# Optimization experiments

Hardware: AMD Instinct MI355X
Metric: run time of the kernel (lower is better)

Reference implementation:

```python
import jax, jax.numpy as jnp
import numpy as np

NUM_EXPERTS = 8
TOP_K = 2
HIDDEN = 2048
INTER = 1408
NUM_TOKENS = 8192


def setup_inputs() -> dict:
    key = jax.random.key(0)
    k1, k2, k3, k4 = jax.random.split(key, 4)
    hidden_states = jax.random.normal(k1, (NUM_TOKENS, HIDDEN), dtype=jnp.float32)
    router_weight = jax.random.normal(k2, (NUM_EXPERTS, HIDDEN), dtype=jnp.float32) * 0.02
    gate_up_proj = jax.random.normal(k3, (NUM_EXPERTS, 2 * INTER, HIDDEN), dtype=jnp.float32) * 0.02
    down_proj = jax.random.normal(k4, (NUM_EXPERTS, HIDDEN, INTER), dtype=jnp.float32) * 0.02
    return {
        "hidden_states": hidden_states,
        "router_weight": router_weight,
        "gate_up_proj": gate_up_proj,
        "down_proj": down_proj,
    }


def reference(hidden_states, router_weight, gate_up_proj, down_proj):
    T, H = hidden_states.shape
    E = router_weight.shape[0]
    dtype = hidden_states.dtype

    # Router: logits -> fp32 softmax -> top-k -> normalize -> cast back
    logits = hidden_states @ router_weight.T                      # [T, E]
    probs = jax.nn.softmax(logits.astype(jnp.float32), axis=-1)
    rw, sel = jax.lax.top_k(probs, TOP_K)                          # [T, K]
    rw = rw / jnp.sum(rw, axis=-1, keepdims=True)                  # norm_topk_prob=True
    rw = rw.astype(dtype)

    # Dense combine weights per token per expert (zero for unselected experts)
    combine = jnp.zeros((T, E), dtype=dtype)
    combine = combine.at[jnp.arange(T)[:, None], sel].add(rw)      # [T, E]

    out = jnp.zeros_like(hidden_states)
    for e in range(E):  # small fixed loop over experts
        gate_up = hidden_states @ gate_up_proj[e].T                # [T, 2I]
        gate, up = jnp.split(gate_up, 2, axis=-1)
        h = jax.nn.silu(gate) * up                                 # SiluAndMul
        expert_out = h @ down_proj[e].T                            # [T, H]
        out = out + combine[:, e:e + 1] * expert_out
    return out
```

## Files before the change

### kernel.cpp

```cpp
#include <hip/hip_runtime.h>
#include <hip/hip_bf16.h>
#include <stdint.h>
#include <math.h>


#define E_ 8
#define H_ 2048
#define I_ 1408
#define T_ 8192
#define NSLOT (T_ * 2)
#define NBLK 64
#define G1S 408
#define G2S 272
#define G1 (8 * G1S)
#define G2 (8 * G2S)

typedef __bf16 bf16;
typedef bf16 bf16x4 __attribute__((ext_vector_type(4)));
typedef bf16 bf16x8 __attribute__((ext_vector_type(8)));
typedef float f32x4 __attribute__((ext_vector_type(4)));

__device__ inline void gl2lds16(const void* g, void* l) {
  __builtin_amdgcn_global_load_lds(
      (const __attribute__((address_space(1))) unsigned int*)g,
      (__attribute__((address_space(3))) unsigned int*)l, 16, 0, 0);
}

__global__ __launch_bounds__(256) void cvtw_k(const float* __restrict__ a, int n8a,
                                              const float* __restrict__ b, int n8b,
                                              bf16* __restrict__ oa,
                                              bf16* __restrict__ ob) {
  int stride = gridDim.x * blockDim.x;
  int ntot = n8a + n8b;
  for (int i = blockIdx.x * blockDim.x + threadIdx.x; i < ntot; i += stride) {
    const float* src; bf16* dst; int k;
    if (i < n8a) { src = a; dst = oa; k = i; }
    else         { src = b; dst = ob; k = i - n8a; }
    const float4* p = (const float4*)src + (size_t)k * 2;
    float4 x = p[0], y = p[1];
    bf16x8 o;
    o[0] = (bf16)x.x; o[1] = (bf16)x.y; o[2] = (bf16)x.z; o[3] = (bf16)x.w;
    o[4] = (bf16)y.x; o[5] = (bf16)y.y; o[6] = (bf16)y.z; o[7] = (bf16)y.w;
    *((bf16x8*)dst + k) = o;
  }
}

__global__ __launch_bounds__(256) void router_k(const float* __restrict__ X,
                                                const float* __restrict__ R,
                                                bf16* __restrict__ xbf,
                                                int* __restrict__ sel,
                                                float* __restrict__ wts) {
  int lane = threadIdx.x & 63;
  int t = blockIdx.x * 4 + (threadIdx.x >> 6);
  const float4* x4 = (const float4*)(X + (size_t)t * H_);
  bf16x4* xb4 = (bf16x4*)(xbf + (size_t)t * H_);
  float acc[E_];
#pragma unroll
  for (int e = 0; e < E_; ++e) acc[e] = 0.f;
#pragma unroll
  for (int i = 0; i < H_ / 256; ++i) {
    float4 x = x4[i * 64 + lane];
    bf16x4 xo; xo[0] = (bf16)x.x; xo[1] = (bf16)x.y; xo[2] = (bf16)x.z; xo[3] = (bf16)x.w;
    xb4[i * 64 + lane] = xo;
#pragma unroll
    for (int e = 0; e < E_; ++e) {
      float4 r = ((const float4*)(R + (size_t)e * H_))[i * 64 + lane];
      acc[e] += x.x * r.x + x.y * r.y + x.z * r.z + x.w * r.w;
    }
  }
#pragma unroll
  for (int e = 0; e < E_; ++e)
#pragma unroll
    for (int off = 32; off > 0; off >>= 1) acc[e] += __shfl_xor(acc[e], off);
  if (lane == 0) {
    int e1 = 0; float l1 = acc[0];
#pragma unroll
    for (int e = 1; e < E_; ++e) if (acc[e] > l1) { l1 = acc[e]; e1 = e; }
    int e2 = -1; float l2 = -3.4e38f;
#pragma unroll
    for (int e = 0; e < E_; ++e) if (e != e1 && acc[e] > l2) { l2 = acc[e]; e2 = e; }
    float d = expf(l2 - l1);
    float inv = 1.f / (1.f + d);
    sel[2 * t] = e1; sel[2 * t + 1] = e2;
    wts[2 * t] = inv; wts[2 * t + 1] = d * inv;
  }
}

__global__ __launch_bounds__(256) void count_k(const int* __restrict__ sel,
                                               int* __restrict__ blockHist) {
  __shared__ int h[E_];
  int t = threadIdx.x;
  if (t < E_) h[t] = 0;
  __syncthreads();
  atomicAdd(&h[sel[blockIdx.x * 256 + t]], 1);
  __syncthreads();
  if (t < E_) blockHist[blockIdx.x * E_ + t] = h[t];
}

__global__ __launch_bounds__(256) void plan_k(const int* __restrict__ blockHist,
                                              int* __restrict__ ctl,
                                              int* __restrict__ blockBase,
                                              int* __restrict__ tm1,
                                              int* __restrict__ tm2) {
  __shared__ int cnts[E_], offs[E_], nm8[E_];
  __shared__ int ps1[22 * E_], ps2[16 * E_];
  int t = threadIdx.x;
  if (t < E_) {
    int c = 0;
    for (int b = 0; b < NBLK; ++b) c += blockHist[b * E_ + t];
    cnts[t] = c; ctl[t] = c;
  }
  __syncthreads();
  if (t == 0) {
    int off = 0;
    for (int e = 0; e < E_; ++e) {
      offs[e] = off; ctl[8 + e] = off; off += cnts[e];
      nm8[e] = (cnts[e] + 127) >> 7;
    }
    int cur1[8] = {0, 0, 0, 0, 0, 0, 0, 0};
    for (int pid = 0; pid < 22 * E_; ++pid) {
      int j = pid >> 3, e = pid & 7, x = (e + j) & 7;
      ps1[pid] = cur1[x]; cur1[x] += nm8[e];
    }
    int cur2[8] = {0, 0, 0, 0, 0, 0, 0, 0};
    for (int pid = 0; pid < 16 * E_; ++pid) {
      int n = pid >> 3, e = pid & 7, x = (e + n) & 7;
      ps2[pid] = cur2[x]; cur2[x] += nm8[e];
    }
  }
  __syncthreads();
  if (t < E_) {
    int run = offs[t];
    for (int b = 0; b < NBLK; ++b) {
      blockBase[b * E_ + t] = run;
      run += blockHist[b * E_ + t];
    }
  }
  for (int pid = t; pid < 22 * E_; pid += 256) {
    int j = pid >> 3, e = pid & 7, x = (e + j) & 7;
    for (int m = 0; m < nm8[e]; ++m)
      tm1[x + 8 * (ps1[pid] + m)] = (e << 16) | (j << 8) | m;
  }
  for (int pid = t; pid < 16 * E_; pid += 256) {
    int n = pid >> 3, e = pid & 7, x = (e + n) & 7;
    for (int m = 0; m < nm8[e]; ++m)
      tm2[x + 8 * (ps2[pid] + m)] = (e << 16) | (n << 8) | m;
  }
}

__global__ __launch_bounds__(256) void scatter_k(const int* __restrict__ sel,
                                                 const float* __restrict__ wts,
                                                 const int* __restrict__ blockBase,
                                                 int* __restrict__ tok,
                                                 float* __restrict__ sw,
                                                 int* __restrict__ inv) {
  __shared__ int wcnt[4][E_];
  int t = threadIdx.x;
  int lane = t & 63, w = t >> 6;
  int i = blockIdx.x * 256 + t;
  int e = sel[i];
  unsigned long long below = (lane == 63) ? ~0ull >> 1 : (1ull << lane) - 1;
  int myrank = 0;
#pragma unroll
  for (int e0 = 0; e0 < E_; ++e0) {
    unsigned long long m = __ballot(e == e0);
    if (e == e0) myrank = __popcll(m & below);
    if (lane == 0) wcnt[w][e0] = __popcll(m);
  }
  __syncthreads();
  int pos = blockBase[blockIdx.x * E_ + e] + myrank;
#pragma unroll
  for (int w2 = 0; w2 < 3; ++w2)
    if (w2 < w) pos += wcnt[w2][e];
  tok[pos] = i >> 1;
  sw[pos] = wts[i];
  inv[i] = pos;
}

__global__ __launch_bounds__(256, 2) void gemm1_k(const bf16* __restrict__ Xb,
                                                  const bf16* __restrict__ Wgu,
                                                  const int* __restrict__ ctl,
                                                  const int* __restrict__ tok,
                                                  const int* __restrict__ tmap,
                                                  bf16* __restrict__ act) {
  const int ent = tmap[blockIdx.x];
  if (ent < 0) return;
  const int e = ent >> 16;
  const int j0 = ((ent >> 8) & 255) * 64;
  const int m0 = (ent & 255) * 128;
  const int cnt = ctl[e];
  const int base = ctl[8 + e];

  __shared__ alignas(16) bf16 lA[2][128 * 64];
  __shared__ alignas(16) bf16 lBg[2][64 * 64];
  __shared__ alignas(16) bf16 lBu[2][64 * 64];

  const int t = threadIdx.x;
  const int lane = t & 63;
  const int wr = (t >> 7) & 1;
  const int wc = (t >> 6) & 1;
  const int lo = lane & 15, hi = lane >> 4;
  const bf16* wg = Wgu + (size_t)e * (2 * I_) * H_;

  const bf16* asrc[4]; int aoff[4];
#pragma unroll
  for (int c = 0; c < 4; ++c) {
    int L = c * 256 + t;
    int row = L >> 3, cc = (L & 7) ^ (row & 7);
    int r = m0 + row; if (r >= cnt) r = cnt - 1;
    asrc[c] = Xb + (size_t)tok[base + r] * H_ + cc * 8;
    aoff[c] = L * 16;
  }
  const bf16* gsrc[2]; const bf16* usrc[2]; int boff[2];
#pragma unroll
  for (int c = 0; c < 2; ++c) {
    int L = c * 256 + t;
    int row = L >> 3, cc = (L & 7) ^ (row & 7);
    gsrc[c] = wg + (size_t)(j0 + row) * H_ + cc * 8;
    usrc[c] = wg + (size_t)(I_ + j0 + row) * H_ + cc * 8;
    boff[c] = L * 16;
  }

#define STG1(b, k)                                                \
  {                                                               \
    _Pragma("unroll")                                             \
    for (int c = 0; c < 4; ++c)                                   \
      gl2lds16(asrc[c] + (k), (char*)lA[b] + aoff[c]);            \
    _Pragma("unroll")                                             \
    for (int c = 0; c < 2; ++c) {                                 \
      gl2lds16(gsrc[c] + (k), (char*)lBg[b] + boff[c]);           \
      gl2lds16(usrc[c] + (k), (char*)lBu[b] + boff[c]);           \
    }                                                             \
  }

  f32x4 zero = {0.f, 0.f, 0.f, 0.f};
  f32x4 ag[4][2], au[4][2];
#pragma unroll
  for (int m = 0; m < 4; ++m)
#pragma unroll
    for (int n = 0; n < 2; ++n) { ag[m][n] = zero; au[m][n] = zero; }

  STG1(0, 0);
  __syncthreads();

  for (int k0 = 0; k0 < H_; k0 += 128) {
#pragma unroll
    for (int p = 0; p < 2; ++p) {
      const int kc = k0 + p * 64;
      if (kc + 64 < H_) STG1(p ^ 1, kc + 64);
#pragma unroll
      for (int kk = 0; kk < 2; ++kk) {
        const int chunk = kk * 4 + hi;
        bf16x8 af[4], bg[2], bu[2];
#pragma unroll
        for (int m = 0; m < 4; ++m) {
          int row = wr * 64 + m * 16 + lo;
          af[m] = *(const bf16x8*)((const char*)lA[p] + row * 128 + ((chunk ^ (row & 7)) * 16));
        }
#pragma unroll
        for (int n = 0; n < 2; ++n) {
          int row = wc * 32 + n * 16 + lo;
          int sw2 = (chunk ^ (row & 7)) * 16;
          bg[n] = *(const bf16x8*)((const char*)lBg[p] + row * 128 + sw2);
          bu[n] = *(const bf16x8*)((const char*)lBu[p] + row * 128 + sw2);
        }
#pragma unroll
        for (int m = 0; m < 4; ++m)
#pragma unroll
          for (int n = 0; n < 2; ++n) {
            ag[m][n] = __builtin_amdgcn_mfma_f32_16x16x32_bf16(af[m], bg[n], ag[m][n], 0, 0, 0);
            au[m][n] = __builtin_amdgcn_mfma_f32_16x16x32_bf16(af[m], bu[n], au[m][n], 0, 0, 0);
          }
      }
      __syncthreads();
    }
  }
#undef STG1

#pragma unroll
  for (int m = 0; m < 4; ++m)
#pragma unroll
    for (int r = 0; r < 4; ++r) {
      int row = m0 + wr * 64 + m * 16 + hi * 4 + r;
      if (row < cnt) {
        bf16* dst = act + (size_t)(base + row) * I_ + j0 + wc * 32 + lo;
#pragma unroll
        for (int n = 0; n < 2; ++n) {
          float g = ag[m][n][r], u = au[m][n][r];
          dst[n * 16] = (bf16)(g / (1.f + __expf(-g)) * u);
        }
      }
    }
}

__global__ __launch_bounds__(256, 2) void gemm2_k(const bf16* __restrict__ act,
                                                  const bf16* __restrict__ Wd,
                                                  const int* __restrict__ ctl,
                                                  const float* __restrict__ sw,
                                                  const int* __restrict__ tmap,
                                                  bf16* __restrict__ y) {
  const int ent = tmap[blockIdx.x];
  if (ent < 0) return;
  const int e = ent >> 16;
  const int n0 = ((ent >> 8) & 255) * 128;
  const int m0 = (ent & 255) * 128;
  const int cnt = ctl[e];
  const int base = ctl[8 + e];

  __shared__ alignas(16) bf16 lA[2][128 * 64];
  __shared__ alignas(16) bf16 lB[2][128 * 64];

  const int t = threadIdx.x;
  const int lane = t & 63;
  const int wr = (t >> 7) & 1;
  const int wc = (t >> 6) & 1;
  const int lo = lane & 15, hi = lane >> 4;
  const bf16* wd = Wd + (size_t)e * H_ * I_;

  const bf16* asrc[4]; int aoff[4];
#pragma unroll
  for (int c = 0; c < 4; ++c) {
    int L = c * 256 + t;
    int row = L >> 3, cc = (L & 7) ^ (row & 7);
    int r = m0 + row; if (r >= cnt) r = cnt - 1;
    asrc[c] = act + (size_t)(base + r) * I_ + cc * 8;
    aoff[c] = L * 16;
  }
  const bf16* bsrc[4]; int boff[4];
#pragma unroll
  for (int c = 0; c < 4; ++c) {
    int L = c * 256 + t;
    int row = L >> 3, cc = (L & 7) ^ (row & 7);
    bsrc[c] = wd + (size_t)(n0 + row) * I_ + cc * 8;
    boff[c] = L * 16;
  }

#define STG2(b, k)                                                \
  {                                                               \
    _Pragma("unroll")                                             \
    for (int c = 0; c < 4; ++c)                                   \
      gl2lds16(asrc[c] + (k), (char*)lA[b] + aoff[c]);            \
    _Pragma("unroll")                                             \
    for (int c = 0; c < 4; ++c)                                   \
      gl2lds16(bsrc[c] + (k), (char*)lB[b] + boff[c]);            \
  }

  f32x4 zero = {0.f, 0.f, 0.f, 0.f};
  f32x4 acc[4][4];
#pragma unroll
  for (int m = 0; m < 4; ++m)
#pragma unroll
    for (int n = 0; n < 4; ++n) acc[m][n] = zero;

  STG2(0, 0);
  __syncthreads();

  for (int k0 = 0; k0 < I_; k0 += 128) {
#pragma unroll
    for (int p = 0; p < 2; ++p) {
      const int kc = k0 + p * 64;
      if (kc + 64 < I_) STG2(p ^ 1, kc + 64);
#pragma unroll
      for (int kk = 0; kk < 2; ++kk) {
        const int chunk = kk * 4 + hi;
        bf16x8 af[4], bb[4];
#pragma unroll
        for (int m = 0; m < 4; ++m) {
          int row = wr * 64 + m * 16 + lo;
          af[m] = *(const bf16x8*)((const char*)lA[p] + row * 128 + ((chunk ^ (row & 7)) * 16));
        }
#pragma unroll
        for (int n = 0; n < 4; ++n) {
          int row = wc * 64 + n * 16 + lo;
          bb[n] = *(const bf16x8*)((const char*)lB[p] + row * 128 + ((chunk ^ (row & 7)) * 16));
        }
#pragma unroll
        for (int m = 0; m < 4; ++m)
#pragma unroll
          for (int n = 0; n < 4; ++n)
            acc[m][n] = __builtin_amdgcn_mfma_f32_16x16x32_bf16(af[m], bb[n], acc[m][n], 0, 0, 0);
      }
      __syncthreads();
    }
  }
#undef STG2

#pragma unroll
  for (int m = 0; m < 4; ++m)
#pragma unroll
    for (int r = 0; r < 4; ++r) {
      int row = m0 + wr * 64 + m * 16 + hi * 4 + r;
      if (row < cnt) {
        float w = sw[base + row];
        bf16* dst = y + (size_t)(base + row) * H_ + n0 + wc * 64 + lo;
#pragma unroll
        for (int n = 0; n < 4; ++n) dst[n * 16] = (bf16)(w * acc[m][n][r]);
      }
    }
}

__global__ __launch_bounds__(256) void combine_k(const bf16* __restrict__ y,
                                                 const int* __restrict__ inv,
                                                 float* __restrict__ out) {
  int idx = blockIdx.x * 256 + threadIdx.x;
  int t = idx >> 8;
  int c = idx & 255;
  int i1 = inv[2 * t], i2 = inv[2 * t + 1];
  bf16x8 a = *((const bf16x8*)(y + (size_t)i1 * H_) + c);
  bf16x8 b = *((const bf16x8*)(y + (size_t)i2 * H_) + c);
  float* op = out + (size_t)t * H_ + c * 8;
#pragma unroll
  for (int k = 0; k < 8; ++k) op[k] = (float)a[k] + (float)b[k];
}

extern "C" void kernel_launch(void* const* d_in, const int* in_sizes, int n_in,
                              void* d_out, int out_size, void* d_ws, size_t ws_size,
                              hipStream_t stream) {
  const float* X = (const float*)d_in[0];
  const float* R = (const float*)d_in[1];
  const float* Wgu = (const float*)d_in[2];
  const float* Wd = (const float*)d_in[3];
  float* out = (float*)d_out;

  char* ws = (char*)d_ws;
  size_t o = 0;
  auto alloc = [&](size_t sz) { void* p = ws + o; o += (sz + 255) & ~(size_t)255; return p; };
  bf16* wgu_bf = (bf16*)alloc(sizeof(bf16) * (size_t)E_ * 2 * I_ * H_);
  bf16* wd_bf  = (bf16*)alloc(sizeof(bf16) * (size_t)E_ * H_ * I_);
  bf16* xbf    = (bf16*)alloc(sizeof(bf16) * (size_t)T_ * H_);
  bf16* actb   = (bf16*)alloc(sizeof(bf16) * (size_t)NSLOT * I_);
  int* sel     = (int*)alloc(4 * NSLOT);
  float* wts   = (float*)alloc(4 * NSLOT);
  int* tokb    = (int*)alloc(4 * NSLOT);
  float* swb   = (float*)alloc(4 * NSLOT);
  int* invb    = (int*)alloc(4 * NSLOT);
  int* ctl     = (int*)alloc(4 * 32);
  int* bh      = (int*)alloc(4 * NBLK * E_);
  int* bb      = (int*)alloc(4 * NBLK * E_);
  int* tm1     = (int*)alloc(4 * G1);
  int* tm2     = (int*)alloc(4 * G2);
  bf16* yb = wgu_bf;

  hipMemsetAsync(tm1, 0xFF, 4 * G1, stream);
  hipMemsetAsync(tm2, 0xFF, 4 * G2, stream);

  cvtw_k<<<2048, 256, 0, stream>>>(Wgu, (int)((size_t)E_ * 2 * I_ * H_ / 8),
                                   Wd, (int)((size_t)E_ * H_ * I_ / 8),
                                   wgu_bf, wd_bf);
  router_k<<<T_ / 4, 256, 0, stream>>>(X, R, xbf, sel, wts);
  count_k<<<NBLK, 256, 0, stream>>>(sel, bh);
  plan_k<<<1, 256, 0, stream>>>(bh, ctl, bb, tm1, tm2);
  scatter_k<<<NBLK, 256, 0, stream>>>(sel, wts, bb, tokb, swb, invb);
  gemm1_k<<<G1, 256, 0, stream>>>(xbf, wgu_bf, ctl, tokb, tm1, actb);
  gemm2_k<<<G2, 256, 0, stream>>>(actb, wd_bf, ctl, swb, tm2, yb);
  combine_k<<<T_ * H_ / 2048, 256, 0, stream>>>(yb, invb, out);
}
```

Before: 602.3 us.

## Retile grouped GEMMs to 256x64 tiles and drop precomputed tile maps

Both expert GEMMs move from 128x128 tiles (2x2 warp grid) to 256-row by 64-column tiles with four warps stacked along M. Weight tiles are reused across more tokens per load, and gate/up rows are interleaved in one B buffer. The tile-map build in plan_k and its memsets are removed. Blocks now decode expert, m and n directly from blockIdx with an expert-interleaved order and exit early when past the expert's token count. This cuts weight traffic and planning overhead, but launches many empty blocks and doubles A-tile LDS use, which may lower occupancy.

```diff
diff --git a/kernel.cpp b/kernel.cpp
--- a/kernel.cpp
+++ b/kernel.cpp
@@ -10,10 +10,11 @@
 #define T_ 8192
 #define NSLOT (T_ * 2)
 #define NBLK 64
-#define G1S 408
-#define G2S 272
-#define G1 (8 * G1S)
-#define G2 (8 * G2S)
+#define NMB 32
+#define NJ1 44
+#define NJ2 32
+#define G1 (NJ1 * NMB * E_)
+#define G2 (NJ2 * NMB * E_)
 
 typedef __bf16 bf16;
 typedef bf16 bf16x4 __attribute__((ext_vector_type(4)));
@@ -97,13 +98,10 @@
   if (t < E_) blockHist[blockIdx.x * E_ + t] = h[t];
 }
 
-__global__ __launch_bounds__(256) void plan_k(const int* __restrict__ blockHist,
-                                              int* __restrict__ ctl,
-                                              int* __restrict__ blockBase,
-                                              int* __restrict__ tm1,
-                                              int* __restrict__ tm2) {
-  __shared__ int cnts[E_], offs[E_], nm8[E_];
-  __shared__ int ps1[22 * E_], ps2[16 * E_];
+__global__ __launch_bounds__(64) void plan_k(const int* __restrict__ blockHist,
+                                             int* __restrict__ ctl,
+                                             int* __restrict__ blockBase) {
+  __shared__ int cnts[E_], offs[E_];
   int t = threadIdx.x;
   if (t < E_) {
     int c = 0;
@@ -113,20 +111,7 @@
   __syncthreads();
   if (t == 0) {
     int off = 0;
-    for (int e = 0; e < E_; ++e) {
-      offs[e] = off; ctl[8 + e] = off; off += cnts[e];
-      nm8[e] = (cnts[e] + 127) >> 7;
-    }
-    int cur1[8] = {0, 0, 0, 0, 0, 0, 0, 0};
-    for (int pid = 0; pid < 22 * E_; ++pid) {
-      int j = pid >> 3, e = pid & 7, x = (e + j) & 7;
-      ps1[pid] = cur1[x]; cur1[x] += nm8[e];
-    }
-    int cur2[8] = {0, 0, 0, 0, 0, 0, 0, 0};
-    for (int pid = 0; pid < 16 * E_; ++pid) {
-      int n = pid >> 3, e = pid & 7, x = (e + n) & 7;
-      ps2[pid] = cur2[x]; cur2[x] += nm8[e];
-    }
+    for (int e = 0; e < E_; ++e) { offs[e] = off; ctl[8 + e] = off; off += cnts[e]; }
   }
   __syncthreads();
   if (t < E_) {
@@ -135,16 +120,6 @@
       blockBase[b * E_ + t] = run;
       run += blockHist[b * E_ + t];
     }
-  }
-  for (int pid = t; pid < 22 * E_; pid += 256) {
-    int j = pid >> 3, e = pid & 7, x = (e + j) & 7;
-    for (int m = 0; m < nm8[e]; ++m)
-      tm1[x + 8 * (ps1[pid] + m)] = (e << 16) | (j << 8) | m;
-  }
-  for (int pid = t; pid < 16 * E_; pid += 256) {
-    int n = pid >> 3, e = pid & 7, x = (e + n) & 7;
-    for (int m = 0; m < nm8[e]; ++m)
-      tm2[x + 8 * (ps2[pid] + m)] = (e << 16) | (n << 8) | m;
   }
 }
 
@@ -181,64 +156,62 @@
                                                   const bf16* __restrict__ Wgu,
                                                   const int* __restrict__ ctl,
                                                   const int* __restrict__ tok,
-                                                  const int* __restrict__ tmap,
                                                   bf16* __restrict__ act) {
-  const int ent = tmap[blockIdx.x];
-  if (ent < 0) return;
-  const int e = ent >> 16;
-  const int j0 = ((ent >> 8) & 255) * 64;
-  const int m0 = (ent & 255) * 128;
+  const int L0 = ((int)blockIdx.x & 7) * (NJ1 * NMB) + ((int)blockIdx.x >> 3);
+  const int e = L0 / (NJ1 * NMB);
+  const int rem = L0 - e * (NJ1 * NMB);
+  const int m0 = (rem / NJ1) * 256;
+  const int j0 = (rem % NJ1) * 32;
   const int cnt = ctl[e];
+  if (m0 >= cnt) return;
   const int base = ctl[8 + e];
 
-  __shared__ alignas(16) bf16 lA[2][128 * 64];
-  __shared__ alignas(16) bf16 lBg[2][64 * 64];
-  __shared__ alignas(16) bf16 lBu[2][64 * 64];
+  __shared__ alignas(16) bf16 lA[2][256 * 64];
+  __shared__ alignas(16) bf16 lB[2][64 * 64];
 
   const int t = threadIdx.x;
   const int lane = t & 63;
-  const int wr = (t >> 7) & 1;
-  const int wc = (t >> 6) & 1;
+  const int w = t >> 6;
   const int lo = lane & 15, hi = lane >> 4;
   const bf16* wg = Wgu + (size_t)e * (2 * I_) * H_;
 
-  const bf16* asrc[4]; int aoff[4];
-#pragma unroll
-  for (int c = 0; c < 4; ++c) {
+  const bf16* asrc[8]; int aoff[8];
+#pragma unroll
+  for (int c = 0; c < 8; ++c) {
     int L = c * 256 + t;
     int row = L >> 3, cc = (L & 7) ^ (row & 7);
     int r = m0 + row; if (r >= cnt) r = cnt - 1;
     asrc[c] = Xb + (size_t)tok[base + r] * H_ + cc * 8;
     aoff[c] = L * 16;
   }
-  const bf16* gsrc[2]; const bf16* usrc[2]; int boff[2];
+  const bf16* bsrc[2]; int boff[2];
 #pragma unroll
   for (int c = 0; c < 2; ++c) {
     int L = c * 256 + t;
     int row = L >> 3, cc = (L & 7) ^ (row & 7);
-    gsrc[c] = wg + (size_t)(j0 + row) * H_ + cc * 8;
-    usrc[c] = wg + (size_t)(I_ + j0 + row) * H_ + cc * 8;
+    int g = row >> 4;
+    int jglob = j0 + (g >> 1) * 16 + (row & 15);
+    const bf16* bb = wg + (size_t)(((g & 1) ? I_ : 0) + jglob) * H_;
+    bsrc[c] = bb + cc * 8;
     boff[c] = L * 16;
   }
 
 #define STG1(b, k)                                                \
   {                                                               \
     _Pragma("unroll")                                             \
-    for (int c = 0; c < 4; ++c)                                   \
+    for (int c = 0; c < 8; ++c)                                   \
       gl2lds16(asrc[c] + (k), (char*)lA[b] + aoff[c]);            \
     _Pragma("unroll")                                             \
-    for (int c = 0; c < 2; ++c) {                                 \
-      gl2lds16(gsrc[c] + (k), (char*)lBg[b] + boff[c]);           \
-      gl2lds16(usrc[c] + (k), (char*)lBu[b] + boff[c]);           \
-    }                                                             \
+    for (int c = 0; c < 2; ++c)                                   \
+      gl2lds16(bsrc[c] + (k), (char*)lB[b] + boff[c]);            \
   }
 
   f32x4 zero = {0.f, 0.f, 0.f, 0.f};
-  f32x4 ag[4][2], au[4][2];
+  f32x4 acc[4][4];
 #pragma unroll
   for (int m = 0; m < 4; ++m)
 #pragma unroll
-    for (int n = 0; n < 2; ++n) { ag[m][n] = zero; au[m][n] = zero; }
+    for (int n = 0; n < 4; ++n) acc[m][n] = zero;
 
   STG1(0, 0);
   __syncthreads();
@@ -251,26 +224,22 @@
 #pragma unroll
       for (int kk = 0; kk < 2; ++kk) {
         const int chunk = kk * 4 + hi;
-        bf16x8 af[4], bg[2], bu[2];
+        bf16x8 af[4], bf[4];
 #pragma unroll
         for (int m = 0; m < 4; ++m) {
-          int row = wr * 64 + m * 16 + lo;
+          int row = w * 64 + m * 16 + lo;
           af[m] = *(const bf16x8*)((const char*)lA[p] + row * 128 + ((chunk ^ (row & 7)) * 16));
         }
 #pragma unroll
-        for (int n = 0; n < 2; ++n) {
-          int row = wc * 32 + n * 16 + lo;
-          int sw2 = (chunk ^ (row & 7)) * 16;
-          bg[n] = *(const bf16x8*)((const char*)lBg[p] + row * 128 + sw2);
-          bu[n] = *(const bf16x8*)((const char*)lBu[p] + row * 128 + sw2);
+        for (int n = 0; n < 4; ++n) {
+          int row = n * 16 + lo;
+          bf[n] = *(const bf16x8*)((const char*)lB[p] + row * 128 + ((chunk ^ (row & 7)) * 16));
         }
 #pragma unroll
         for (int m = 0; m < 4; ++m)
 #pragma unroll
-          for (int n = 0; n < 2; ++n) {
-            ag[m][n] = __builtin_amdgcn_mfma_f32_16x16x32_bf16(af[m], bg[n], ag[m][n], 0, 0, 0);
-            au[m][n] = __builtin_amdgcn_mfma_f32_16x16x32_bf16(af[m], bu[n], au[m][n], 0, 0, 0);
-          }
+          for (int n = 0; n < 4; ++n)
+            acc[m][n] = __builtin_amdgcn_mfma_f32_16x16x32_bf16(af[m], bf[n], acc[m][n], 0, 0, 0);
       }
       __syncthreads();
     }
@@ -281,13 +250,13 @@
   for (int m = 0; m < 4; ++m)
 #pragma unroll
     for (int r = 0; r < 4; ++r) {
-      int row = m0 + wr * 64 + m * 16 + hi * 4 + r;
+      int row = m0 + w * 64 + m * 16 + hi * 4 + r;
       if (row < cnt) {
-        bf16* dst = act + (size_t)(base + row) * I_ + j0 + wc * 32 + lo;
-#pragma unroll
-        for (int n = 0; n < 2; ++n) {
-          float g = ag[m][n][r], u = au[m][n][r];
-          dst[n * 16] = (bf16)(g / (1.f + __expf(-g)) * u);
+        bf16* dst = act + (size_t)(base + row) * I_ + j0;
+#pragma unroll
+        for (int p = 0; p < 2; ++p) {
+          float g = acc[m][2 * p][r], u = acc[m][2 * p + 1][r];
+          dst[p * 16 + lo] = (bf16)(g / (1.f + __expf(-g)) * u);
         }
       }
     }
@@ -297,38 +266,37 @@
                                                   const bf16* __restrict__ Wd,
                                                   const int* __restrict__ ctl,
                                                   const float* __restrict__ sw,
-                                                  const int* __restrict__ tmap,
                                                   bf16* __restrict__ y) {
-  const int ent = tmap[blockIdx.x];
-  if (ent < 0) return;
-  const int e = ent >> 16;
-  const int n0 = ((ent >> 8) & 255) * 128;
-  const int m0 = (ent & 255) * 128;
+  const int L0 = ((int)blockIdx.x & 7) * (NJ2 * NMB) + ((int)blockIdx.x >> 3);
+  const int e = L0 / (NJ2 * NMB);
+  const int rem = L0 - e * (NJ2 * NMB);
+  const int m0 = (rem / NJ2) * 256;
+  const int n0 = (rem % NJ2) * 64;
   const int cnt = ctl[e];
+  if (m0 >= cnt) return;
   const int base = ctl[8 + e];
 
-  __shared__ alignas(16) bf16 lA[2][128 * 64];
-  __shared__ alignas(16) bf16 lB[2][128 * 64];
+  __shared__ alignas(16) bf16 lA[2][256 * 64];
+  __shared__ alignas(16) bf16 lB[2][64 * 64];
 
   const int t = threadIdx.x;
   const int lane = t & 63;
-  const int wr = (t >> 7) & 1;
-  const int wc = (t >> 6) & 1;
+  const int w = t >> 6;
   const int lo = lane & 15, hi = lane >> 4;
   const bf16* wd = Wd + (size_t)e * H_ * I_;
 
-  const bf16* asrc[4]; int aoff[4];
-#pragma unroll
-  for (int c = 0; c < 4; ++c) {
+  const bf16* asrc[8]; int aoff[8];
+#pragma unroll
+  for (int c = 0; c < 8; ++c) {
     int L = c * 256 + t;
     int row = L >> 3, cc = (L & 7) ^ (row & 7);
     int r = m0 + row; if (r >= cnt) r = cnt - 1;
     asrc[c] = act + (size_t)(base + r) * I_ + cc * 8;
     aoff[c] = L * 16;
   }
-  const bf16* bsrc[4]; int boff[4];
-#pragma unroll
-  for (int c = 0; c < 4; ++c) {
+  const bf16* bsrc[2]; int boff[2];
+#pragma unroll
+  for (int c = 0; c < 2; ++c) {
     int L = c * 256 + t;
     int row = L >> 3, cc = (L & 7) ^ (row & 7);
     bsrc[c] = wd + (size_t)(n0 + row) * I_ + cc * 8;
@@ -338,10 +306,10 @@
 #define STG2(b, k)                                                \
   {                                                               \
     _Pragma("unroll")                                             \
-    for (int c = 0; c < 4; ++c)                                   \
+    for (int c = 0; c < 8; ++c)                                   \
       gl2lds16(asrc[c] + (k), (char*)lA[b] + aoff[c]);            \
     _Pragma("unroll")                                             \
-    for (int c = 0; c < 4; ++c)                                   \
+    for (int c = 0; c < 2; ++c)                                   \
       gl2lds16(bsrc[c] + (k), (char*)lB[b] + boff[c]);            \
   }
 
@@ -363,22 +331,22 @@
 #pragma unroll
       for (int kk = 0; kk < 2; ++kk) {
         const int chunk = kk * 4 + hi;
-        bf16x8 af[4], bb[4];
+        bf16x8 af[4], bf[4];
 #pragma unroll
         for (int m = 0; m < 4; ++m) {
-          int row = wr * 64 + m * 16 + lo;
+          int row = w * 64 + m * 16 + lo;
           af[m] = *(const bf16x8*)((const char*)lA[p] + row * 128 + ((chunk ^ (row & 7)) * 16));
         }
 #pragma unroll
         for (int n = 0; n < 4; ++n) {
-          int row = wc * 64 + n * 16 + lo;
-          bb[n] = *(const bf16x8*)((const char*)lB[p] + row * 128 + ((chunk ^ (row & 7)) * 16));
+          int row = n * 16 + lo;
+          bf[n] = *(const bf16x8*)((const char*)lB[p] + row * 128 + ((chunk ^ (row & 7)) * 16));
         }
 #pragma unroll
         for (int m = 0; m < 4; ++m)
 #pragma unroll
           for (int n = 0; n < 4; ++n)
-            acc[m][n] = __builtin_amdgcn_mfma_f32_16x16x32_bf16(af[m], bb[n], acc[m][n], 0, 0, 0);
+            acc[m][n] = __builtin_amdgcn_mfma_f32_16x16x32_bf16(af[m], bf[n], acc[m][n], 0, 0, 0);
       }
       __syncthreads();
     }
@@ -389,12 +357,12 @@
   for (int m = 0; m < 4; ++m)
 #pragma unroll
     for (int r = 0; r < 4; ++r) {
-      int row = m0 + wr * 64 + m * 16 + hi * 4 + r;
+      int row = m0 + w * 64 + m * 16 + hi * 4 + r;
       if (row < cnt) {
-        float w = sw[base + row];
-        bf16* dst = y + (size_t)(base + row) * H_ + n0 + wc * 64 + lo;
-#pragma unroll
-        for (int n = 0; n < 4; ++n) dst[n * 16] = (bf16)(w * acc[m][n][r]);
+        float wgt = sw[base + row];
+        bf16* dst = y + (size_t)(base + row) * H_ + n0;
+#pragma unroll
+        for (int n = 0; n < 4; ++n) dst[n * 16 + lo] = (bf16)(wgt * acc[m][n][r]);
       }
     }
 }
@@ -437,21 +405,16 @@
   int* ctl     = (int*)alloc(4 * 32);
   int* bh      = (int*)alloc(4 * NBLK * E_);
   int* bb      = (int*)alloc(4 * NBLK * E_);
-  int* tm1     = (int*)alloc(4 * G1);
-  int* tm2     = (int*)alloc(4 * G2);
   bf16* yb = wgu_bf;
-
-  hipMemsetAsync(tm1, 0xFF, 4 * G1, stream);
-  hipMemsetAsync(tm2, 0xFF, 4 * G2, stream);
 
   cvtw_k<<<2048, 256, 0, stream>>>(Wgu, (int)((size_t)E_ * 2 * I_ * H_ / 8),
                                    Wd, (int)((size_t)E_ * H_ * I_ / 8),
                                    wgu_bf, wd_bf);
   router_k<<<T_ / 4, 256, 0, stream>>>(X, R, xbf, sel, wts);
   count_k<<<NBLK, 256, 0, stream>>>(sel, bh);
-  plan_k<<<1, 256, 0, stream>>>(bh, ctl, bb, tm1, tm2);
+  plan_k<<<1, 64, 0, stream>>>(bh, ctl, bb);
   scatter_k<<<NBLK, 256, 0, stream>>>(sel, wts, bb, tokb, swb, invb);
-  gemm1_k<<<G1, 256, 0, stream>>>(xbf, wgu_bf, ctl, tokb, tm1, actb);
-  gemm2_k<<<G2, 256, 0, stream>>>(actb, wd_bf, ctl, swb, tm2, yb);
+  gemm1_k<<<G1, 256, 0, stream>>>(xbf, wgu_bf, ctl, tokb, actb);
+  gemm2_k<<<G2, 256, 0, stream>>>(actb, wd_bf, ctl, swb, yb);
   combine_k<<<T_ * H_ / 2048, 256, 0, stream>>>(yb, invb, out);
 }
```

Result: no change. 609.2 us (+1.1%).

## Replace precomputed tile map with full static grid and early-exit blocks

Applied to the files above, without the earlier changes.

Removes the tile-map construction in the planning kernel and the memsets that cleared it. The GEMMs now launch a grid sized for the worst case per expert, decoding expert, row tile and column tile from an interleaved block index and exiting when the row tile exceeds the expert's token count. This drops serial planning work and two memset launches, but launches many blocks that return immediately. It also drops the two-blocks-per-CU occupancy hint.

```diff
diff --git a/kernel.cpp b/kernel.cpp
--- a/kernel.cpp
+++ b/kernel.cpp
@@ -10,10 +10,6 @@
 #define T_ 8192
 #define NSLOT (T_ * 2)
 #define NBLK 64
-#define G1S 408
-#define G2S 272
-#define G1 (8 * G1S)
-#define G2 (8 * G2S)
 
 typedef __bf16 bf16;
 typedef bf16 bf16x4 __attribute__((ext_vector_type(4)));
@@ -97,13 +93,10 @@
   if (t < E_) blockHist[blockIdx.x * E_ + t] = h[t];
 }
 
-__global__ __launch_bounds__(256) void plan_k(const int* __restrict__ blockHist,
-                                              int* __restrict__ ctl,
-                                              int* __restrict__ blockBase,
-                                              int* __restrict__ tm1,
-                                              int* __restrict__ tm2) {
-  __shared__ int cnts[E_], offs[E_], nm8[E_];
-  __shared__ int ps1[22 * E_], ps2[16 * E_];
+__global__ __launch_bounds__(64) void plan_k(const int* __restrict__ blockHist,
+                                             int* __restrict__ ctl,
+                                             int* __restrict__ blockBase) {
+  __shared__ int cnts[E_], offs[E_];
   int t = threadIdx.x;
   if (t < E_) {
     int c = 0;
@@ -113,20 +106,7 @@
   __syncthreads();
   if (t == 0) {
     int off = 0;
-    for (int e = 0; e < E_; ++e) {
-      offs[e] = off; ctl[8 + e] = off; off += cnts[e];
-      nm8[e] = (cnts[e] + 127) >> 7;
-    }
-    int cur1[8] = {0, 0, 0, 0, 0, 0, 0, 0};
-    for (int pid = 0; pid < 22 * E_; ++pid) {
-      int j = pid >> 3, e = pid & 7, x = (e + j) & 7;
-      ps1[pid] = cur1[x]; cur1[x] += nm8[e];
-    }
-    int cur2[8] = {0, 0, 0, 0, 0, 0, 0, 0};
-    for (int pid = 0; pid < 16 * E_; ++pid) {
-      int n = pid >> 3, e = pid & 7, x = (e + n) & 7;
-      ps2[pid] = cur2[x]; cur2[x] += nm8[e];
-    }
+    for (int e = 0; e < E_; ++e) { offs[e] = off; ctl[8 + e] = off; off += cnts[e]; }
   }
   __syncthreads();
   if (t < E_) {
@@ -135,16 +115,6 @@
       blockBase[b * E_ + t] = run;
       run += blockHist[b * E_ + t];
     }
-  }
-  for (int pid = t; pid < 22 * E_; pid += 256) {
-    int j = pid >> 3, e = pid & 7, x = (e + j) & 7;
-    for (int m = 0; m < nm8[e]; ++m)
-      tm1[x + 8 * (ps1[pid] + m)] = (e << 16) | (j << 8) | m;
-  }
-  for (int pid = t; pid < 16 * E_; pid += 256) {
-    int n = pid >> 3, e = pid & 7, x = (e + n) & 7;
-    for (int m = 0; m < nm8[e]; ++m)
-      tm2[x + 8 * (ps2[pid] + m)] = (e << 16) | (n << 8) | m;
   }
 }
 
@@ -177,18 +147,21 @@
   inv[i] = pos;
 }
 
-__global__ __launch_bounds__(256, 2) void gemm1_k(const bf16* __restrict__ Xb,
-                                                  const bf16* __restrict__ Wgu,
-                                                  const int* __restrict__ ctl,
-                                                  const int* __restrict__ tok,
-                                                  const int* __restrict__ tmap,
-                                                  bf16* __restrict__ act) {
-  const int ent = tmap[blockIdx.x];
-  if (ent < 0) return;
-  const int e = ent >> 16;
-  const int j0 = ((ent >> 8) & 255) * 64;
-  const int m0 = (ent & 255) * 128;
+__global__ __launch_bounds__(256) void gemm1_k(const bf16* __restrict__ Xb,
+                                               const bf16* __restrict__ Wgu,
+                                               const int* __restrict__ ctl,
+                                               const int* __restrict__ tok,
+                                               bf16* __restrict__ act) {
+  constexpr int NJ = I_ / 64;
+  constexpr int NM = T_ / 128;
+  constexpr int NB = NJ * NM * E_;
+  const int L0 = ((int)blockIdx.x & 7) * (NB >> 3) + ((int)blockIdx.x >> 3);
+  const int e = L0 / (NJ * NM);
+  const int rem = L0 - e * (NJ * NM);
+  const int m0 = (rem / NJ) * 128;
+  const int j0 = (rem % NJ) * 64;
   const int cnt = ctl[e];
+  if (m0 >= cnt) return;
   const int base = ctl[8 + e];
 
   __shared__ alignas(16) bf16 lA[2][128 * 64];
@@ -293,18 +266,21 @@
     }
 }
 
-__global__ __launch_bounds__(256, 2) void gemm2_k(const bf16* __restrict__ act,
-                                                  const bf16* __restrict__ Wd,
-                                                  const int* __restrict__ ctl,
-                                                  const float* __restrict__ sw,
-                                                  const int* __restrict__ tmap,
-                                                  bf16* __restrict__ y) {
-  const int ent = tmap[blockIdx.x];
-  if (ent < 0) return;
-  const int e = ent >> 16;
-  const int n0 = ((ent >> 8) & 255) * 128;
-  const int m0 = (ent & 255) * 128;
+__global__ __launch_bounds__(256) void gemm2_k(const bf16* __restrict__ act,
+                                               const bf16* __restrict__ Wd,
+                                               const int* __restrict__ ctl,
+                                               const float* __restrict__ sw,
+                                               bf16* __restrict__ y) {
+  constexpr int NJ = H_ / 128;
+  constexpr int NM = T_ / 128;
+  constexpr int NB = NJ * NM * E_;
+  const int L0 = ((int)blockIdx.x & 7) * (NB >> 3) + ((int)blockIdx.x >> 3);
+  const int e = L0 / (NJ * NM);
+  const int rem = L0 - e * (NJ * NM);
+  const int m0 = (rem / NJ) * 128;
+  const int n0 = (rem % NJ) * 128;
   const int cnt = ctl[e];
+  if (m0 >= cnt) return;
   const int base = ctl[8 + e];
 
   __shared__ alignas(16) bf16 lA[2][128 * 64];
@@ -437,21 +413,16 @@
   int* ctl     = (int*)alloc(4 * 32);
   int* bh      = (int*)alloc(4 * NBLK * E_);
   int* bb      = (int*)alloc(4 * NBLK * E_);
-  int* tm1     = (int*)alloc(4 * G1);
-  int* tm2     = (int*)alloc(4 * G2);
   bf16* yb = wgu_bf;
-
-  hipMemsetAsync(tm1, 0xFF, 4 * G1, stream);
-  hipMemsetAsync(tm2, 0xFF, 4 * G2, stream);
 
   cvtw_k<<<2048, 256, 0, stream>>>(Wgu, (int)((size_t)E_ * 2 * I_ * H_ / 8),
                                    Wd, (int)((size_t)E_ * H_ * I_ / 8),
                                    wgu_bf, wd_bf);
   router_k<<<T_ / 4, 256, 0, stream>>>(X, R, xbf, sel, wts);
   count_k<<<NBLK, 256, 0, stream>>>(sel, bh);
-  plan_k<<<1, 256, 0, stream>>>(bh, ctl, bb, tm1, tm2);
+  plan_k<<<1, 64, 0, stream>>>(bh, ctl, bb);
   scatter_k<<<NBLK, 256, 0, stream>>>(sel, wts, bb, tokb, swb, invb);
-  gemm1_k<<<G1, 256, 0, stream>>>(xbf, wgu_bf, ctl, tokb, tm1, actb);
-  gemm2_k<<<G2, 256, 0, stream>>>(actb, wd_bf, ctl, swb, tm2, yb);
+  gemm1_k<<<(I_ / 64) * (T_ / 128) * E_, 256, 0, stream>>>(xbf, wgu_bf, ctl, tokb, actb);
+  gemm2_k<<<(H_ / 128) * (T_ / 128) * E_, 256, 0, stream>>>(actb, wd_bf, ctl, swb, yb);
   combine_k<<<T_ * H_ / 2048, 256, 0, stream>>>(yb, invb, out);
 }
```

New measurement: 519.3 us (median of 2 runs). -13.8%, faster.
